# Kernel optimization log

Measured on AMD Instinct MI355X. Metric: run time of the kernel, lower is better.

Reference implementation:

```python
import jax, jax.numpy as jnp
import numpy as np

STUDENT_FRAMES = [0, 2, 4, 6]
EXTRA_FRAMES = [1, 3, 5, 7]       # teacher-only frames, sorted
SHARED_T = [2, 4, 6]              # shared frames in teacher indexing
SHARED_S = [1, 2, 3]              # same frames in student indexing
TOPK = 4
EPS = 1e-8                        # eps of _cos_angle's F.normalize
HUBER_DELTA = 1.0
A1 = A2 = A3 = 1.0


def _huber(pred, target, delta=HUBER_DELTA):
    err = pred - target
    ae = jnp.abs(err)
    return jnp.where(ae <= delta, 0.5 * err * err, delta * (ae - 0.5 * delta))


def _angles(h, r, c):
    """Cosine angles for the triangle (shared=h [B,F,S,D], ref=r [B,R,D], sim=c [B,R,K,D]).
    Expands cos(a-b, c-b) via pairwise dot products so no [.,.,.,.,D] tensor is materialized.
    Returns (a1, a2, a3) each of shape [B,F,R,S,K]."""
    ss = jnp.einsum('bfsd,brkd->bfrsk', h, c)   # shared . sim
    sr = jnp.einsum('bfsd,brd->bfrs', h, r)     # shared . ref
    rk = jnp.einsum('brd,brkd->brk', r, c)      # ref . sim
    rr = jnp.sum(r * r, -1)                     # [B,R]
    kk = jnp.sum(c * c, -1)                     # [B,R,K]
    hh = jnp.sum(h * h, -1)                     # [B,F,S]
    sr_ = sr[..., None]                         # bfrs1
    rk_ = rk[:, None, :, None, :]               # b1r1k
    rr_ = rr[:, None, :, None, None]            # b1r11
    kk_ = kk[:, None, :, None, :]               # b1r1k
    hh_ = hh[:, :, None, :, None]               # bf1s1
    n_hr = jnp.sqrt(jnp.maximum(hh_ + rr_ - 2.0 * sr_, 0.0))  # ||shared-ref||
    n_cr = jnp.sqrt(jnp.maximum(kk_ + rr_ - 2.0 * rk_, 0.0))  # ||sim-ref||
    n_hc = jnp.sqrt(jnp.maximum(hh_ + kk_ - 2.0 * ss, 0.0))   # ||shared-sim||
    def cos(num, na, nb):
        return num / (jnp.maximum(na, EPS) * jnp.maximum(nb, EPS))
    a1 = cos(ss - sr_ - rk_ + rr_, n_hr, n_cr)  # cos(shared-ref, sim-ref)
    a2 = cos(sr_ - rk_ - ss + kk_, n_cr, n_hc)  # cos(ref-sim, shared-sim)
    a3 = cos(rk_ - sr_ - ss + hh_, n_hr, n_hc)  # cos(ref-shared, sim-shared)
    return a1, a2, a3


def setup_inputs() -> dict:
    key = jax.random.key(0)
    k1, k2, k3, k4 = jax.random.split(key, 4)
    B, V, P, D = 4, 8, 1369, 2048
    teacher_feats = jax.random.normal(k1, (B, V, P, D), jnp.float32)
    student_feats = jax.random.normal(k2, (B, len(STUDENT_FRAMES), P, D), jnp.float32)
    ref_perm = jax.random.permutation(k3, P)[:128].astype(jnp.int32)
    shared_perm = jax.random.permutation(k4, P)[:128].astype(jnp.int32)
    return {'teacher_feats': teacher_feats, 'student_feats': student_feats,
            'ref_perm': ref_perm, 'shared_perm': shared_perm}


def reference(teacher_feats, student_feats, ref_perm, shared_perm):
    teacher = jax.lax.stop_gradient(teacher_feats)  # teacher side is fully detached
    B, V, P, D = teacher.shape

    ref_t = teacher[:, STUDENT_FRAMES[0], ref_perm, :]        # [B,R,D]
    ref_s = student_feats[:, 0, ref_perm, :]                  # [B,R,D]

    # extra (teacher-only) frames concatenated along patches -> [B, 4*P, D]
    extra_t = teacher[:, jnp.array(EXTRA_FRAMES)].reshape(B, len(EXTRA_FRAMES) * P, D)

    # cosine similarity + topk selection (selection_mode='topk')
    ref_tn = ref_t / jnp.maximum(jnp.linalg.norm(ref_t, axis=-1, keepdims=True), 1e-12)
    extra_tn = extra_t / jnp.maximum(jnp.linalg.norm(extra_t, axis=-1, keepdims=True), 1e-12)
    sim = jnp.einsum('brd,bed->bre', ref_tn, extra_tn)        # [B,R,4P]
    _, idx = jax.lax.top_k(sim, TOPK)                         # [B,R,K]
    sim_high = jax.vmap(lambda e, i: e[i])(extra_t, idx)      # [B,R,K,D]

    shared_t = teacher[:, jnp.array(SHARED_T)][:, :, shared_perm, :]        # [B,F,S,D]
    shared_s = student_feats[:, jnp.array(SHARED_S)][:, :, shared_perm, :]  # [B,F,S,D]

    a1_t, a2_t, a3_t = _angles(shared_t, ref_t, sim_high)
    a1_s, a2_s, a3_s = _angles(shared_s, ref_s, sim_high)

    l1 = _huber(a1_s, a1_t).mean()
    l2 = _huber(a2_s, a2_t).mean()
    l3 = _huber(a3_s, a3_t).mean()
    loss = A1 * l1 + A2 * l2 + A3 * l3
    return loss
```

## Files before the change

### kernel.cpp

```cpp
#include <hip/hip_runtime.h>

#define B_ 4
#define V_ 8
#define P_ 1369
#define D_ 2048
#define R_ 128
#define F_ 3
#define K_ 4
#define E_ 5476
#define CAND_ 8
#define EPS_ 1e-8f
#define ETILES_ 86
#define SIMBLK_ (ETILES_*B_*2)

typedef unsigned short u16;
typedef __attribute__((ext_vector_type(8))) short bf16x8;
typedef __attribute__((ext_vector_type(4))) float f32x4;

__device__ inline u16 f2bf(float f){
  unsigned int u = __float_as_uint(f);
  u = u + 0x7fffu + ((u >> 16) & 1u);
  return (u16)(u >> 16);
}
__device__ inline int pack2bf(float lo, float hi){
  return (int)(((unsigned)f2bf(hi) << 16) | (unsigned)f2bf(lo));
}
__device__ inline float sq8(float4 a, float4 b){
  return a.x*a.x + a.y*a.y + a.z*a.z + a.w*a.w
       + b.x*b.x + b.y*b.y + b.z*b.z + b.w*b.w;
}
__device__ inline float huber1(float e){
  float ae = fabsf(e);
  return ae <= 1.0f ? 0.5f*e*e : (ae - 0.5f);
}
__device__ inline float blk_sum(float v, float* scr){
  for (int off = 32; off; off >>= 1) v += __shfl_xor(v, off, 64);
  __syncthreads();
  if ((threadIdx.x & 63) == 0) scr[threadIdx.x >> 6] = v;
  __syncthreads();
  float s = scr[0] + scr[1] + scr[2] + scr[3];
  __syncthreads();
  return s;
}

__global__ __launch_bounds__(256) void k_prep_ref(
    const float* __restrict__ teacher, const float* __restrict__ student,
    const int* __restrict__ ref_perm,
    u16* __restrict__ ref_tn, float* __restrict__ rr_t, float* __restrict__ rr_s){
  __shared__ float scr[4];
  int br = blockIdx.x, b = br >> 7, r = br & 127, t = threadIdx.x;
  int p = ref_perm[r];
  const float* tp = teacher + ((size_t)(b*V_)*P_ + p)*D_;
  const float* sp = student + ((size_t)(b*4)*P_ + p)*D_;
  float4 x0 = *(const float4*)(tp + t*8);
  float4 x1 = *(const float4*)(tp + t*8 + 4);
  float sumt = blk_sum(sq8(x0, x1), scr);
  float4 y0 = *(const float4*)(sp + t*8);
  float4 y1 = *(const float4*)(sp + t*8 + 4);
  float sums = blk_sum(sq8(y0, y1), scr);
  if (t == 0){ rr_t[br] = sumt; rr_s[br] = sums; }
  float inv = 1.0f / fmaxf(sqrtf(sumt), 1e-12f);
  int4 pt = { pack2bf(x0.x*inv, x0.y*inv), pack2bf(x0.z*inv, x0.w*inv),
              pack2bf(x1.x*inv, x1.y*inv), pack2bf(x1.z*inv, x1.w*inv) };
  *(int4*)(ref_tn + (size_t)br*D_ + t*8) = pt;
}

__global__ __launch_bounds__(256) void k_sim_fused(
    const float* __restrict__ teacher, const float* __restrict__ student,
    const u16* __restrict__ ref_tn, const int* __restrict__ shared_perm,
    float* __restrict__ simPart, float* __restrict__ nsqPart,
    u16* __restrict__ shT, u16* __restrict__ shS,
    float* __restrict__ hhT, float* __restrict__ hhS){
  __shared__ __align__(16) u16 As[128][72];
  __shared__ __align__(16) u16 Bs[64][72];
  __shared__ float scr4[4];
  int bx = blockIdx.x, t = threadIdx.x;
  if (bx < SIMBLK_){
    int h = bx / (ETILES_*B_);
    int rem = bx % (ETILES_*B_);
    int b = rem / ETILES_, et = rem % ETILES_;
    int e0 = et * 64;
    int lane = t & 63, w = t >> 6, wm = w >> 1, wn = w & 1;
    f32x4 acc[4][2];
    for (int i = 0; i < 4; i++)
      for (int j = 0; j < 2; j++)
        acc[i][j] = (f32x4){0.f, 0.f, 0.f, 0.f};
    int arow = t >> 1, acol = (t & 1) * 32;
    int brow = t >> 2, bcol = (t & 3) * 16;
    int e = e0 + brow;
    const u16* asrc = ref_tn + ((size_t)(b*128 + arow))*D_ + acol;
    const float* bsrc = nullptr;
    if (e < E_) bsrc = teacher + ((size_t)(b*V_ + 1 + 2*(e / P_))*P_ + (e % P_))*D_ + bcol;
    float q = 0.0f;
    int lr = lane & 15;
    int kbeg = h * 1024, kend = kbeg + 1024;
    for (int k0 = kbeg; k0 < kend; k0 += 64){
      __syncthreads();
#pragma unroll
      for (int u = 0; u < 4; u++)
        *(int4*)&As[arow][acol + u*8] = *(const int4*)(asrc + k0 + u*8);
      float4 z0, z1, z2, z3;
      if (bsrc){
        z0 = *(const float4*)(bsrc + k0);      z1 = *(const float4*)(bsrc + k0 + 4);
        z2 = *(const float4*)(bsrc + k0 + 8);  z3 = *(const float4*)(bsrc + k0 + 12);
      } else {
        z0 = make_float4(0.f,0.f,0.f,0.f); z1 = z0; z2 = z0; z3 = z0;
      }
      q += sq8(z0, z1) + sq8(z2, z3);
      int4 p0 = { pack2bf(z0.x, z0.y), pack2bf(z0.z, z0.w),
                  pack2bf(z1.x, z1.y), pack2bf(z1.z, z1.w) };
      int4 p1 = { pack2bf(z2.x, z2.y), pack2bf(z2.z, z2.w),
                  pack2bf(z3.x, z3.y), pack2bf(z3.z, z3.w) };
      *(int4*)&Bs[brow][bcol]     = p0;
      *(int4*)&Bs[brow][bcol + 8] = p1;
      __syncthreads();
#pragma unroll
      for (int kk = 0; kk < 2; kk++){
        int kof = kk*32 + (lane >> 4) * 8;
        bf16x8 bf0 = *(const bf16x8*)&Bs[wn*32 + lr][kof];
        bf16x8 bf1 = *(const bf16x8*)&Bs[wn*32 + 16 + lr][kof];
#pragma unroll
        for (int mi = 0; mi < 4; mi++){
          bf16x8 af = *(const bf16x8*)&As[wm*64 + mi*16 + lr][kof];
          acc[mi][0] = __builtin_amdgcn_mfma_f32_16x16x32_bf16(af, bf0, acc[mi][0], 0, 0, 0);
          acc[mi][1] = __builtin_amdgcn_mfma_f32_16x16x32_bf16(af, bf1, acc[mi][1], 0, 0, 0);
        }
      }
    }
    q += __shfl_xor(q, 1, 64);
    q += __shfl_xor(q, 2, 64);
    if ((t & 3) == 0 && e < E_) nsqPart[(size_t)(h*4 + b)*E_ + e] = q;
    int lg = lane >> 4;
#pragma unroll
    for (int mi = 0; mi < 4; mi++){
#pragma unroll
      for (int ni = 0; ni < 2; ni++){
        int el = wn*32 + ni*16 + lr;
        int e_idx = e0 + el;
        if (e_idx < E_){
#pragma unroll
          for (int reg = 0; reg < 4; reg++){
            int r_idx = wm*64 + mi*16 + lg*4 + reg;
            simPart[((size_t)((h*4 + b)*128 + r_idx))*E_ + e_idx] = acc[mi][ni][reg];
          }
        }
      }
    }
  } else {
    int id = bx - SIMBLK_;
    int b = id / 384, fs = id % 384;
    int f = fs >> 7, s = fs & 127;
    int p = shared_perm[s];
    const float* tp = teacher + ((size_t)(b*V_ + 2 + 2*f)*P_ + p)*D_;
    const float* sp = student + ((size_t)(b*4 + 1 + f)*P_ + p)*D_;
    float4 x0 = *(const float4*)(tp + t*8);
    float4 x1 = *(const float4*)(tp + t*8 + 4);
    float sumt = blk_sum(sq8(x0, x1), scr4);
    int4 pt = { pack2bf(x0.x, x0.y), pack2bf(x0.z, x0.w),
                pack2bf(x1.x, x1.y), pack2bf(x1.z, x1.w) };
    *(int4*)(shT + (size_t)id*D_ + t*8) = pt;
    float4 y0 = *(const float4*)(sp + t*8);
    float4 y1 = *(const float4*)(sp + t*8 + 4);
    float sums = blk_sum(sq8(y0, y1), scr4);
    int4 ps = { pack2bf(y0.x, y0.y), pack2bf(y0.z, y0.w),
                pack2bf(y1.x, y1.y), pack2bf(y1.z, y1.w) };
    *(int4*)(shS + (size_t)id*D_ + t*8) = ps;
    if (t == 0){ hhT[id] = sumt; hhS[id] = sums; }
  }
}

__global__ __launch_bounds__(256) void k_rescore(
    const float* __restrict__ teacher, const float* __restrict__ student,
    const int* __restrict__ ref_perm,
    const float* __restrict__ simPart, const float* __restrict__ nsqPart,
    const float* __restrict__ rr_t,
    u16* __restrict__ packT, u16* __restrict__ packS,
    float* __restrict__ kkw, float* __restrict__ rkT, float* __restrict__ rkS){
  __shared__ float v[E_];
  __shared__ float rT[D_];
  __shared__ float rS[D_];
  __shared__ float tv[256];
  __shared__ int   ti[256];
  __shared__ float rv[4];
  __shared__ int ri[4];
  __shared__ int cand[CAND_];
  __shared__ float csim[CAND_], cq[CAND_], cdT[CAND_];
  __shared__ int order[4];
  int br = blockIdx.x, b = br >> 7, r = br & 127, t = threadIdx.x;
  int lane = t & 63, w = t >> 6;
  const float* p0 = simPart + ((size_t)(b*128 + r))*E_;
  const float* p1 = simPart + ((size_t)((4 + b)*128 + r))*E_;
  const float* q0 = nsqPart + (size_t)b*E_;
  const float* q1 = nsqPart + (size_t)(4 + b)*E_;
  for (int i = t; i < E_; i += 256){
    float qq = q0[i] + q1[i];
    float inv = 1.0f / fmaxf(sqrtf(qq), 1e-12f);
    v[i] = (p0[i] + p1[i]) * inv;
  }
  __syncthreads();
  {
    float bv = -3.4e38f; int bi = 0x7fffffff;
    for (int i = t; i < E_; i += 256){
      float x = v[i];
      if (x > bv){ bv = x; bi = i; }
    }
    tv[t] = bv; ti[t] = bi;
  }
  __syncthreads();
  for (int c = 0; c < CAND_; c++){
    float mv = tv[t]; int mi2 = ti[t];
    for (int off = 32; off; off >>= 1){
      float ov = __shfl_down(mv, off, 64);
      int   oi = __shfl_down(mi2, off, 64);
      if (ov > mv || (ov == mv && oi < mi2)){ mv = ov; mi2 = oi; }
    }
    if (lane == 0){ rv[w] = mv; ri[w] = mi2; }
    __syncthreads();
    if (t == 0){
      for (int w2 = 1; w2 < 4; w2++)
        if (rv[w2] > rv[0] || (rv[w2] == rv[0] && ri[w2] < ri[0])){ rv[0] = rv[w2]; ri[0] = ri[w2]; }
      cand[c] = ri[0];
      v[ri[0]] = -3.4e38f;
    }
    __syncthreads();
    int win = cand[c];
    if (t == (win & 255)){
      float nb = -3.4e38f; int nbi = 0x7fffffff;
      for (int i = t; i < E_; i += 256){
        float x = v[i];
        if (x > nb){ nb = x; nbi = i; }
      }
      tv[t] = nb; ti[t] = nbi;
    }
    __syncthreads();
  }
  int p = ref_perm[r];
  const float* tp = teacher + ((size_t)(b*V_)*P_ + p)*D_;
  const float* sp = student + ((size_t)(b*4)*P_ + p)*D_;
  float4 x0 = *(const float4*)(tp + t*8);
  float4 x1 = *(const float4*)(tp + t*8 + 4);
  float4 y0 = *(const float4*)(sp + t*8);
  float4 y1 = *(const float4*)(sp + t*8 + 4);
  *(float4*)&rT[t*8]   = x0; *(float4*)&rT[t*8+4] = x1;
  *(float4*)&rS[t*8]   = y0; *(float4*)&rS[t*8+4] = y1;
  {
    int4 pt = { pack2bf(x0.x, x0.y), pack2bf(x0.z, x0.w),
                pack2bf(x1.x, x1.y), pack2bf(x1.z, x1.w) };
    *(int4*)(packT + ((size_t)(br*5 + 4))*D_ + t*8) = pt;
    int4 ps = { pack2bf(y0.x, y0.y), pack2bf(y0.z, y0.w),
                pack2bf(y1.x, y1.y), pack2bf(y1.z, y1.w) };
    *(int4*)(packS + ((size_t)(br*5 + 4))*D_ + t*8) = ps;
  }
  float invt = 1.0f / fmaxf(sqrtf(rr_t[br]), 1e-12f);
  __syncthreads();
  for (int c = w; c < CAND_; c += 4){
    int e = cand[c];
    const float* xp = teacher + ((size_t)(b*V_ + 1 + 2*(e / P_))*P_ + (e % P_))*D_;
    float d = 0.f, q = 0.f;
#pragma unroll
    for (int j = 0; j < 32; j++){
      float xv = xp[lane + 64*j];
      d += xv * rT[lane + 64*j];
      q += xv * xv;
    }
    for (int off = 32; off; off >>= 1){
      d += __shfl_xor(d, off, 64);
      q += __shfl_xor(q, off, 64);
    }
    if (lane == 0){
      cdT[c] = d; cq[c] = q;
      csim[c] = d * invt / fmaxf(sqrtf(q), 1e-12f);
    }
  }
  __syncthreads();
  if (t == 0){
    unsigned used = 0;
    for (int k = 0; k < 4; k++){
      int best = -1;
      for (int c = 0; c < CAND_; c++){
        if (used & (1u << c)) continue;
        if (best < 0){ best = c; continue; }
        if (csim[c] > csim[best] ||
            (csim[c] == csim[best] && cand[c] < cand[best])) best = c;
      }
      used |= 1u << best;
      order[k] = best;
    }
  }
  __syncthreads();
  {
    int c = order[w];
    int e = cand[c];
    const float* xp = teacher + ((size_t)(b*V_ + 1 + 2*(e / P_))*P_ + (e % P_))*D_;
    float ds = 0.f;
#pragma unroll
    for (int j = 0; j < 32; j++)
      ds += xp[lane + 64*j] * rS[lane + 64*j];
    for (int off = 32; off; off >>= 1) ds += __shfl_xor(ds, off, 64);
    if (lane == 0){
      kkw[br*4 + w] = cq[c];
      rkT[br*4 + w] = cdT[c];
      rkS[br*4 + w] = ds;
    }
    const float* src = xp + lane*32;
#pragma unroll
    for (int u = 0; u < 4; u++){
      float4 a  = *(const float4*)(src + u*8);
      float4 b2 = *(const float4*)(src + u*8 + 4);
      int4 pc = { pack2bf(a.x, a.y), pack2bf(a.z, a.w),
                  pack2bf(b2.x, b2.y), pack2bf(b2.z, b2.w) };
      size_t po = ((size_t)(br*5 + w))*D_ + lane*32 + u*8;
      *(int4*)(packT + po) = pc;
      *(int4*)(packS + po) = pc;
    }
  }
}

__global__ __launch_bounds__(256) void k_angle_gemm(
    const u16* __restrict__ shT, const u16* __restrict__ shS,
    const u16* __restrict__ packT, const u16* __restrict__ packS,
    float* __restrict__ outT, float* __restrict__ outS){
  __shared__ __align__(16) u16 As[128][72];
  __shared__ __align__(16) u16 Bs[64][72];
  int which = blockIdx.z;
  const u16* A  = which ? shS : shT;
  const u16* Bp = which ? packS : packT;
  float* out = which ? outS : outT;
  int b = blockIdx.y;
  int mt = blockIdx.x % 3, nt = blockIdx.x / 3;
  int m0 = mt*128, n0 = nt*64;
  int t = threadIdx.x, lane = t & 63, w = t >> 6, wm = w >> 1, wn = w & 1;
  f32x4 acc[4][2];
  for (int i = 0; i < 4; i++)
    for (int j = 0; j < 2; j++)
      acc[i][j] = (f32x4){0.f, 0.f, 0.f, 0.f};
  int arow = t >> 1, acol = (t & 1) * 32;
  int brow = t >> 2, bcol = (t & 3) * 16;
  const u16* asrc = A  + ((size_t)(b*384 + m0 + arow))*D_ + acol;
  const u16* bsrc = Bp + ((size_t)(b*640 + n0 + brow))*D_ + bcol;
  int lr = lane & 15;
  for (int k0 = 0; k0 < D_; k0 += 64){
    __syncthreads();
#pragma unroll
    for (int u = 0; u < 4; u++)
      *(int4*)&As[arow][acol + u*8] = *(const int4*)(asrc + k0 + u*8);
    *(int4*)&Bs[brow][bcol]     = *(const int4*)(bsrc + k0);
    *(int4*)&Bs[brow][bcol + 8] = *(const int4*)(bsrc + k0 + 8);
    __syncthreads();
#pragma unroll
    for (int kk = 0; kk < 2; kk++){
      int kof = kk*32 + (lane >> 4) * 8;
      bf16x8 bf0 = *(const bf16x8*)&Bs[wn*32 + lr][kof];
      bf16x8 bf1 = *(const bf16x8*)&Bs[wn*32 + 16 + lr][kof];
#pragma unroll
      for (int mi = 0; mi < 4; mi++){
        bf16x8 af = *(const bf16x8*)&As[wm*64 + mi*16 + lr][kof];
        acc[mi][0] = __builtin_amdgcn_mfma_f32_16x16x32_bf16(af, bf0, acc[mi][0], 0, 0, 0);
        acc[mi][1] = __builtin_amdgcn_mfma_f32_16x16x32_bf16(af, bf1, acc[mi][1], 0, 0, 0);
      }
    }
  }
  int lg = lane >> 4;
#pragma unroll
  for (int mi = 0; mi < 4; mi++)
#pragma unroll
    for (int ni = 0; ni < 2; ni++)
#pragma unroll
      for (int reg = 0; reg < 4; reg++){
        int r_idx = wm*64 + mi*16 + lg*4 + reg;
        int c_idx = wn*32 + ni*16 + lr;
        out[((size_t)(b*384 + m0 + r_idx))*640 + n0 + c_idx] = acc[mi][ni][reg];
      }
}

__global__ __launch_bounds__(256) void k_assemble(
    const float* __restrict__ outT, const float* __restrict__ outS,
    const float* __restrict__ hhT, const float* __restrict__ hhS,
    const float* __restrict__ rrT, const float* __restrict__ rrS,
    const float* __restrict__ kkw, const float* __restrict__ rkT, const float* __restrict__ rkS,
    double* __restrict__ partials){
  __shared__ double dscr[4];
  int idx = blockIdx.x*256 + threadIdx.x;
  int r = idx & 127, s = (idx >> 7) & 127, bf = idx >> 14;
  int f = bf % 3, b = bf / 3;
  int fs = f*128 + s;
  const float* oT = outT + ((size_t)(b*384 + fs))*640 + r*5;
  const float* oS = outS + ((size_t)(b*384 + fs))*640 + r*5;
  float hh_t = hhT[b*384 + fs], hh_s = hhS[b*384 + fs];
  float rr_tv = rrT[b*128 + r], rr_sv = rrS[b*128 + r];
  float sr_t = oT[4], sr_s = oS[4];
  float nhr_t = sqrtf(fmaxf(hh_t + rr_tv - 2.0f*sr_t, 0.0f));
  float nhr_s = sqrtf(fmaxf(hh_s + rr_sv - 2.0f*sr_s, 0.0f));
  float h1 = 0.f, h2 = 0.f, h3 = 0.f;
#pragma unroll
  for (int k = 0; k < 4; k++){
    float ss_t = oT[k], ss_s = oS[k];
    float kk = kkw[(b*128 + r)*4 + k];
    float rk_t = rkT[(b*128 + r)*4 + k];
    float rk_s = rkS[(b*128 + r)*4 + k];
    float ncr_t = sqrtf(fmaxf(kk + rr_tv - 2.0f*rk_t, 0.0f));
    float ncr_s = sqrtf(fmaxf(kk + rr_sv - 2.0f*rk_s, 0.0f));
    float nhc_t = sqrtf(fmaxf(hh_t + kk - 2.0f*ss_t, 0.0f));
    float nhc_s = sqrtf(fmaxf(hh_s + kk - 2.0f*ss_s, 0.0f));
    float a1t = (ss_t - sr_t - rk_t + rr_tv) / (fmaxf(nhr_t, EPS_) * fmaxf(ncr_t, EPS_));
    float a2t = (sr_t - rk_t - ss_t + kk)    / (fmaxf(ncr_t, EPS_) * fmaxf(nhc_t, EPS_));
    float a3t = (rk_t - sr_t - ss_t + hh_t)  / (fmaxf(nhr_t, EPS_) * fmaxf(nhc_t, EPS_));
    float a1s = (ss_s - sr_s - rk_s + rr_sv) / (fmaxf(nhr_s, EPS_) * fmaxf(ncr_s, EPS_));
    float a2s = (sr_s - rk_s - ss_s + kk)    / (fmaxf(ncr_s, EPS_) * fmaxf(nhc_s, EPS_));
    float a3s = (rk_s - sr_s - ss_s + hh_s)  / (fmaxf(nhr_s, EPS_) * fmaxf(nhc_s, EPS_));
    h1 += huber1(a1s - a1t);
    h2 += huber1(a2s - a2t);
    h3 += huber1(a3s - a3t);
  }
  double d1 = h1, d2 = h2, d3 = h3;
  for (int off = 32; off; off >>= 1){
    d1 += __shfl_xor(d1, off, 64);
    d2 += __shfl_xor(d2, off, 64);
    d3 += __shfl_xor(d3, off, 64);
  }
  int w = threadIdx.x >> 6;
  if ((threadIdx.x & 63) == 0) dscr[w] = d1;
  __syncthreads();
  if (threadIdx.x == 0) partials[blockIdx.x*3 + 0] = dscr[0]+dscr[1]+dscr[2]+dscr[3];
  __syncthreads();
  if ((threadIdx.x & 63) == 0) dscr[w] = d2;
  __syncthreads();
  if (threadIdx.x == 0) partials[blockIdx.x*3 + 1] = dscr[0]+dscr[1]+dscr[2]+dscr[3];
  __syncthreads();
  if ((threadIdx.x & 63) == 0) dscr[w] = d3;
  __syncthreads();
  if (threadIdx.x == 0) partials[blockIdx.x*3 + 2] = dscr[0]+dscr[1]+dscr[2]+dscr[3];
}

__global__ __launch_bounds__(256) void k_final(
    const double* __restrict__ partials, float* __restrict__ out){
  __shared__ double dscr[12];
  int t = threadIdx.x;
  double l1 = 0, l2 = 0, l3 = 0;
  for (int i = t; i < 768; i += 256){
    l1 += partials[i*3 + 0];
    l2 += partials[i*3 + 1];
    l3 += partials[i*3 + 2];
  }
  for (int off = 32; off; off >>= 1){
    l1 += __shfl_xor(l1, off, 64);
    l2 += __shfl_xor(l2, off, 64);
    l3 += __shfl_xor(l3, off, 64);
  }
  int w = t >> 6;
  if ((t & 63) == 0){ dscr[w*3] = l1; dscr[w*3+1] = l2; dscr[w*3+2] = l3; }
  __syncthreads();
  if (t == 0){
    double L1 = dscr[0] + dscr[3] + dscr[6] + dscr[9];
    double L2 = dscr[1] + dscr[4] + dscr[7] + dscr[10];
    double L3 = dscr[2] + dscr[5] + dscr[8] + dscr[11];
    out[0] = (float)((L1 + L2 + L3) / 786432.0);
  }
}

extern "C" void kernel_launch(void* const* d_in, const int* in_sizes, int n_in,
                              void* d_out, int out_size, void* d_ws, size_t ws_size,
                              hipStream_t stream){
  (void)in_sizes; (void)n_in; (void)out_size; (void)ws_size;
  const float* teacher = (const float*)d_in[0];
  const float* student = (const float*)d_in[1];
  const int* ref_perm = (const int*)d_in[2];
  const int* shared_perm = (const int*)d_in[3];
  float* out = (float*)d_out;

  char* ws = (char*)d_ws;
  size_t off = 0;
  auto alloc = [&](size_t bytes)->char*{
    char* pp = ws + off;
    off += (bytes + 255) & ~(size_t)255;
    return pp;
  };
  u16*    ref_tn  = (u16*)   alloc((size_t)B_*R_*D_*sizeof(u16));
  float*  rr_t    = (float*) alloc(B_*R_*sizeof(float));
  float*  rr_s    = (float*) alloc(B_*R_*sizeof(float));
  float*  kkw     = (float*) alloc(B_*R_*K_*sizeof(float));
  float*  rkT     = (float*) alloc(B_*R_*K_*sizeof(float));
  float*  rkS     = (float*) alloc(B_*R_*K_*sizeof(float));
  u16*    shT     = (u16*)   alloc((size_t)B_*384*D_*sizeof(u16));
  u16*    shS     = (u16*)   alloc((size_t)B_*384*D_*sizeof(u16));
  float*  hhT     = (float*) alloc(B_*384*sizeof(float));
  float*  hhS     = (float*) alloc(B_*384*sizeof(float));
  float*  outT    = (float*) alloc((size_t)B_*384*640*sizeof(float));
  float*  outS    = (float*) alloc((size_t)B_*384*640*sizeof(float));
  double* partials= (double*)alloc(768*3*sizeof(double));
  float*  simPart = (float*) alloc((size_t)2*B_*R_*E_*sizeof(float));
  float*  nsqPart = (float*) alloc((size_t)2*B_*E_*sizeof(float));
  u16*    packT   = (u16*)   alloc((size_t)B_*R_*5*D_*sizeof(u16));
  u16*    packS   = (u16*)   alloc((size_t)B_*R_*5*D_*sizeof(u16));

  k_prep_ref<<<dim3(B_*R_), dim3(256), 0, stream>>>(teacher, student, ref_perm,
                                                    ref_tn, rr_t, rr_s);
  k_sim_fused<<<dim3(SIMBLK_ + 1536), dim3(256), 0, stream>>>(
      teacher, student, ref_tn, shared_perm, simPart, nsqPart, shT, shS, hhT, hhS);
  k_rescore<<<dim3(B_*R_), dim3(256), 0, stream>>>(teacher, student, ref_perm,
                                                   simPart, nsqPart, rr_t,
                                                   packT, packS, kkw, rkT, rkS);
  k_angle_gemm<<<dim3(30, B_, 2), dim3(256), 0, stream>>>(shT, shS, packT, packS, outT, outS);
  k_assemble<<<dim3(768), dim3(256), 0, stream>>>(outT, outS, hhT, hhS, rr_t, rr_s, kkw, rkT, rkS, partials);
  k_final<<<dim3(1), dim3(256), 0, stream>>>(partials, out);
}
```

Measured before the change: 133.8 us.

## Prefetch next K tile into registers and split angle GEMM along K

Both MFMA GEMM loops now load the next K-slice from global memory into registers while the current LDS tile is being consumed, so global latency overlaps with compute. The angle GEMM is split into two K halves, which doubles its grid from 240 to 480 blocks to fill more CUs. Each half writes to its own output buffer and the assemble kernel adds the two partial sums. The bf16 packing also switches to the HIP intrinsic. The cost is extra register pressure, twice the output buffer memory, and extra reads in the assemble step.

Measured after the change: 126.4 us. 1.06x faster.

```diff
diff --git a/kernel.cpp b/kernel.cpp
--- a/kernel.cpp
+++ b/kernel.cpp
@@ -1,4 +1,5 @@
 #include <hip/hip_runtime.h>
+#include <hip/hip_bf16.h>
 
 #define B_ 4
 #define V_ 8
@@ -12,18 +13,15 @@
 #define EPS_ 1e-8f
 #define ETILES_ 86
 #define SIMBLK_ (ETILES_*B_*2)
+#define HOFF_ ((size_t)B_*384*640)
 
 typedef unsigned short u16;
 typedef __attribute__((ext_vector_type(8))) short bf16x8;
 typedef __attribute__((ext_vector_type(4))) float f32x4;
 
-__device__ inline u16 f2bf(float f){
-  unsigned int u = __float_as_uint(f);
-  u = u + 0x7fffu + ((u >> 16) & 1u);
-  return (u16)(u >> 16);
-}
 __device__ inline int pack2bf(float lo, float hi){
-  return (int)(((unsigned)f2bf(hi) << 16) | (unsigned)f2bf(lo));
+  __hip_bfloat162 h = __float22bfloat162_rn(make_float2(lo, hi));
+  int r; __builtin_memcpy(&r, &h, 4); return r;
 }
 __device__ inline float sq8(float4 a, float4 b){
   return a.x*a.x + a.y*a.y + a.z*a.z + a.w*a.w
@@ -94,26 +92,39 @@
     float q = 0.0f;
     int lr = lane & 15;
     int kbeg = h * 1024, kend = kbeg + 1024;
+    int4 aa0, aa1, aa2, aa3;
+    float4 za0, za1, za2, za3;
+    {
+      aa0 = *(const int4*)(asrc + kbeg);      aa1 = *(const int4*)(asrc + kbeg + 8);
+      aa2 = *(const int4*)(asrc + kbeg + 16); aa3 = *(const int4*)(asrc + kbeg + 24);
+      if (bsrc){
+        za0 = *(const float4*)(bsrc + kbeg);      za1 = *(const float4*)(bsrc + kbeg + 4);
+        za2 = *(const float4*)(bsrc + kbeg + 8);  za3 = *(const float4*)(bsrc + kbeg + 12);
+      } else { za0 = make_float4(0.f,0.f,0.f,0.f); za1 = za0; za2 = za0; za3 = za0; }
+    }
     for (int k0 = kbeg; k0 < kend; k0 += 64){
       __syncthreads();
-#pragma unroll
-      for (int u = 0; u < 4; u++)
-        *(int4*)&As[arow][acol + u*8] = *(const int4*)(asrc + k0 + u*8);
-      float4 z0, z1, z2, z3;
-      if (bsrc){
-        z0 = *(const float4*)(bsrc + k0);      z1 = *(const float4*)(bsrc + k0 + 4);
-        z2 = *(const float4*)(bsrc + k0 + 8);  z3 = *(const float4*)(bsrc + k0 + 12);
-      } else {
-        z0 = make_float4(0.f,0.f,0.f,0.f); z1 = z0; z2 = z0; z3 = z0;
-      }
-      q += sq8(z0, z1) + sq8(z2, z3);
-      int4 p0 = { pack2bf(z0.x, z0.y), pack2bf(z0.z, z0.w),
-                  pack2bf(z1.x, z1.y), pack2bf(z1.z, z1.w) };
-      int4 p1 = { pack2bf(z2.x, z2.y), pack2bf(z2.z, z2.w),
-                  pack2bf(z3.x, z3.y), pack2bf(z3.z, z3.w) };
+      *(int4*)&As[arow][acol]      = aa0;
+      *(int4*)&As[arow][acol + 8]  = aa1;
+      *(int4*)&As[arow][acol + 16] = aa2;
+      *(int4*)&As[arow][acol + 24] = aa3;
+      q += sq8(za0, za1) + sq8(za2, za3);
+      int4 p0 = { pack2bf(za0.x, za0.y), pack2bf(za0.z, za0.w),
+                  pack2bf(za1.x, za1.y), pack2bf(za1.z, za1.w) };
+      int4 p1 = { pack2bf(za2.x, za2.y), pack2bf(za2.z, za2.w),
+                  pack2bf(za3.x, za3.y), pack2bf(za3.z, za3.w) };
       *(int4*)&Bs[brow][bcol]     = p0;
       *(int4*)&Bs[brow][bcol + 8] = p1;
       __syncthreads();
+      int kn = k0 + 64;
+      if (kn < kend){
+        aa0 = *(const int4*)(asrc + kn);      aa1 = *(const int4*)(asrc + kn + 8);
+        aa2 = *(const int4*)(asrc + kn + 16); aa3 = *(const int4*)(asrc + kn + 24);
+        if (bsrc){
+          za0 = *(const float4*)(bsrc + kn);      za1 = *(const float4*)(bsrc + kn + 4);
+          za2 = *(const float4*)(bsrc + kn + 8);  za3 = *(const float4*)(bsrc + kn + 12);
+        }
+      }
 #pragma unroll
       for (int kk = 0; kk < 2; kk++){
         int kof = kk*32 + (lane >> 4) * 8;
@@ -322,10 +333,10 @@
     float* __restrict__ outT, float* __restrict__ outS){
   __shared__ __align__(16) u16 As[128][72];
   __shared__ __align__(16) u16 Bs[64][72];
-  int which = blockIdx.z;
+  int which = blockIdx.z >> 1, h = blockIdx.z & 1;
   const u16* A  = which ? shS : shT;
   const u16* Bp = which ? packS : packT;
-  float* out = which ? outS : outT;
+  float* out = (which ? outS : outT) + h * HOFF_;
   int b = blockIdx.y;
   int mt = blockIdx.x % 3, nt = blockIdx.x / 3;
   int m0 = mt*128, n0 = nt*64;
@@ -339,14 +350,26 @@
   const u16* asrc = A  + ((size_t)(b*384 + m0 + arow))*D_ + acol;
   const u16* bsrc = Bp + ((size_t)(b*640 + n0 + brow))*D_ + bcol;
   int lr = lane & 15;
-  for (int k0 = 0; k0 < D_; k0 += 64){
+  int kbeg = h * 1024, kend = kbeg + 1024;
+  int4 ra0, ra1, ra2, ra3, rb0, rb1;
+  ra0 = *(const int4*)(asrc + kbeg);      ra1 = *(const int4*)(asrc + kbeg + 8);
+  ra2 = *(const int4*)(asrc + kbeg + 16); ra3 = *(const int4*)(asrc + kbeg + 24);
+  rb0 = *(const int4*)(bsrc + kbeg);      rb1 = *(const int4*)(bsrc + kbeg + 8);
+  for (int k0 = kbeg; k0 < kend; k0 += 64){
     __syncthreads();
-#pragma unroll
-    for (int u = 0; u < 4; u++)
-      *(int4*)&As[arow][acol + u*8] = *(const int4*)(asrc + k0 + u*8);
-    *(int4*)&Bs[brow][bcol]     = *(const int4*)(bsrc + k0);
-    *(int4*)&Bs[brow][bcol + 8] = *(const int4*)(bsrc + k0 + 8);
+    *(int4*)&As[arow][acol]      = ra0;
+    *(int4*)&As[arow][acol + 8]  = ra1;
+    *(int4*)&As[arow][acol + 16] = ra2;
+    *(int4*)&As[arow][acol + 24] = ra3;
+    *(int4*)&Bs[brow][bcol]     = rb0;
+    *(int4*)&Bs[brow][bcol + 8] = rb1;
     __syncthreads();
+    int kn = k0 + 64;
+    if (kn < kend){
+      ra0 = *(const int4*)(asrc + kn);      ra1 = *(const int4*)(asrc + kn + 8);
+      ra2 = *(const int4*)(asrc + kn + 16); ra3 = *(const int4*)(asrc + kn + 24);
+      rb0 = *(const int4*)(bsrc + kn);      rb1 = *(const int4*)(bsrc + kn + 8);
+    }
 #pragma unroll
     for (int kk = 0; kk < 2; kk++){
       int kof = kk*32 + (lane >> 4) * 8;
@@ -384,17 +407,18 @@
   int r = idx & 127, s = (idx >> 7) & 127, bf = idx >> 14;
   int f = bf % 3, b = bf / 3;
   int fs = f*128 + s;
-  const float* oT = outT + ((size_t)(b*384 + fs))*640 + r*5;
-  const float* oS = outS + ((size_t)(b*384 + fs))*640 + r*5;
+  size_t base = ((size_t)(b*384 + fs))*640 + r*5;
+  const float* oT0 = outT + base; const float* oT1 = oT0 + HOFF_;
+  const float* oS0 = outS + base; const float* oS1 = oS0 + HOFF_;
   float hh_t = hhT[b*384 + fs], hh_s = hhS[b*384 + fs];
   float rr_tv = rrT[b*128 + r], rr_sv = rrS[b*128 + r];
-  float sr_t = oT[4], sr_s = oS[4];
+  float sr_t = oT0[4] + oT1[4], sr_s = oS0[4] + oS1[4];
   float nhr_t = sqrtf(fmaxf(hh_t + rr_tv - 2.0f*sr_t, 0.0f));
   float nhr_s = sqrtf(fmaxf(hh_s + rr_sv - 2.0f*sr_s, 0.0f));
   float h1 = 0.f, h2 = 0.f, h3 = 0.f;
 #pragma unroll
   for (int k = 0; k < 4; k++){
-    float ss_t = oT[k], ss_s = oS[k];
+    float ss_t = oT0[k] + oT1[k], ss_s = oS0[k] + oS1[k];
     float kk = kkw[(b*128 + r)*4 + k];
     float rk_t = rkT[(b*128 + r)*4 + k];
     float rk_s = rkS[(b*128 + r)*4 + k];
@@ -485,8 +509,8 @@
   u16*    shS     = (u16*)   alloc((size_t)B_*384*D_*sizeof(u16));
   float*  hhT     = (float*) alloc(B_*384*sizeof(float));
   float*  hhS     = (float*) alloc(B_*384*sizeof(float));
-  float*  outT    = (float*) alloc((size_t)B_*384*640*sizeof(float));
-  float*  outS    = (float*) alloc((size_t)B_*384*640*sizeof(float));
+  float*  outT    = (float*) alloc((size_t)2*B_*384*640*sizeof(float));
+  float*  outS    = (float*) alloc((size_t)2*B_*384*640*sizeof(float));
   double* partials= (double*)alloc(768*3*sizeof(double));
   float*  simPart = (float*) alloc((size_t)2*B_*R_*E_*sizeof(float));
   float*  nsqPart = (float*) alloc((size_t)2*B_*E_*sizeof(float));
@@ -500,7 +524,7 @@
   k_rescore<<<dim3(B_*R_), dim3(256), 0, stream>>>(teacher, student, ref_perm,
                                                    simPart, nsqPart, rr_t,
                                                    packT, packS, kkw, rkT, rkS);
-  k_angle_gemm<<<dim3(30, B_, 2), dim3(256), 0, stream>>>(shT, shS, packT, packS, outT, outS);
+  k_angle_gemm<<<dim3(30, B_, 4), dim3(256), 0, stream>>>(shT, shS, packT, packS, outT, outS);
   k_assemble<<<dim3(768), dim3(256), 0, stream>>>(outT, outS, hhT, hhS, rr_t, rr_s, kkw, rkT, rkS, partials);
   k_final<<<dim3(1), dim3(256), 0, stream>>>(partials, out);
 }
```
